# Kernel optimization log

Hardware: AMD Instinct MI355X
Metric: run time of the kernel (lower is better)

## Reference

```python
import jax, jax.numpy as jnp
import numpy as np

RADIUS = 0.08
NSAMPLE = 32


def setup_inputs() -> dict:
    key = jax.random.key(0)
    k1, k2, k3 = jax.random.split(key, 3)
    xyz = jax.random.uniform(k1, (20000, 3), dtype=jnp.float32)          # (N, 3)
    new_xyz = jax.random.uniform(k2, (2, 2048, 3), dtype=jnp.float32)    # (B, P, 3)
    features = jax.random.normal(k3, (64, 20000), dtype=jnp.float32)     # (C, N)
    return {"xyz": xyz, "new_xyz": new_xyz, "features": features}


def _ball_query(xyz, new_xyz, radius, nsample):
    """Replicates pointnet2 grid ball query.
    Returns idx (B,P,nsample) int32 of the FIRST nsample in-ball point indices
    (in original point order), padded with the first found index (0 if none),
    and idn (B,P,nsample) int32 validity flags (all ones if ball is empty,
    matching the kernel's untouched init of 1).
    """
    xyz = jax.lax.stop_gradient(xyz)
    new_xyz = jax.lax.stop_gradient(new_xyz)
    N = xyz.shape[0]
    # squared distances (B, P, N) via ||a||^2 + ||b||^2 - 2 a.b (no (B,P,N,3) temp)
    x2 = jnp.sum(xyz * xyz, axis=-1)                 # (N,)
    q2 = jnp.sum(new_xyz * new_xyz, axis=-1)         # (B, P)
    cross = jnp.einsum("bpd,nd->bpn", new_xyz, xyz)  # (B, P, N)
    d2 = q2[..., None] + x2[None, None, :] - 2.0 * cross
    mask = d2 < radius * radius                      # (B, P, N)
    # encode "first nsample in-ball indices in ascending point order":
    scores = jnp.where(mask, jnp.arange(N, dtype=jnp.int32), N)
    neg_vals, _ = jax.lax.top_k(-scores, nsample)    # largest of -scores = smallest scores
    cand = -neg_vals                                 # (B, P, nsample), sorted ascending
    valid = cand < N
    first = jnp.where(valid[..., :1], cand[..., :1], 0)
    idx = jnp.where(valid, cand, first).astype(jnp.int32)
    empty = ~valid[..., :1]                          # ball has no neighbors
    idn = jnp.where(valid | empty, 1, 0).astype(jnp.int32)
    return idx, idn


def _group(features, idx):
    """features (C, N), idx (B, P, S) -> (B, C, P, S) gather."""
    g = jnp.take(features, idx, axis=1)              # (C, B, P, S)
    return jnp.transpose(g, (1, 0, 2, 3))


def reference(xyz, new_xyz, features):
    idx, idn = _ball_query(xyz, new_xyz, RADIUS, NSAMPLE)
    grouped_xyz = _group(jnp.transpose(xyz), idx)                    # (B, 3, P, S)
    grouped_xyz = grouped_xyz - jnp.transpose(new_xyz, (0, 2, 1))[..., None]
    grouped_features = _group(features, idx)                         # (B, C, P, S)
    new_features = jnp.concatenate([grouped_xyz, grouped_features], axis=1)
    return new_features, idn
```

## Files before the change

kernel.cpp:

```cpp
#include <hip/hip_runtime.h>
#include <hip/hip_bf16.h>

#define NPTS   20000
#define BATCH  2
#define NQ     2048
#define NS     32
#define NC     64
#define NCOUT  67
#define NQTOT  (BATCH * NQ)
#define NF_ELEMS (BATCH * NCOUT * NQ * NS)

#define GRID   12
#define NCELL  (GRID * GRID * GRID)
#define CAND_CAP 128

__device__ __forceinline__ float sq3(float a, float b, float c) {
    return __fadd_rn(__fadd_rn(__fmul_rn(a, a), __fmul_rn(b, b)), __fmul_rn(c, c));
}

__global__ __launch_bounds__(256) void zero_counts_kernel(int* __restrict__ cnt) {
    const int t = threadIdx.x;
    #pragma unroll
    for (int i = 0; i < 7; ++i) {
        const int c = t * 7 + i;
        if (c < NCELL) cnt[c] = 0;
    }
}

__global__ __launch_bounds__(256) void transpose_count_kernel(
        const float* __restrict__ features, const float* __restrict__ xyz,
        float* __restrict__ featT, int* __restrict__ cellOf,
        int* __restrict__ cnt) {
    __shared__ float tile[64][65];
    const int n0 = blockIdx.x * 64;
    const int t  = threadIdx.x;

    if (t < 64) {
        const int n = n0 + t;
        if (n < NPTS) {
            const float x = xyz[n * 3 + 0];
            const float y = xyz[n * 3 + 1];
            const float z = xyz[n * 3 + 2];
            const int cx = min(max((int)(x * (float)GRID), 0), GRID - 1);
            const int cy = min(max((int)(y * (float)GRID), 0), GRID - 1);
            const int cz = min(max((int)(z * (float)GRID), 0), GRID - 1);
            const int cell = (cx * GRID + cy) * GRID + cz;
            cellOf[n] = cell;
            atomicAdd(&cnt[cell], 1);
        }
    }

    const int nn   = t & 63;
    const int cgrp = t >> 6;
    for (int k = 0; k < 16; ++k) {
        const int cc = cgrp * 16 + k;
        const int n  = n0 + nn;
        if (n < NPTS) tile[cc][nn] = features[cc * NPTS + n];
    }
    __syncthreads();
    const int cc2  = t & 63;
    const int ngrp = t >> 6;
    for (int k = 0; k < 16; ++k) {
        const int nn2 = ngrp * 16 + k;
        const int n   = n0 + nn2;
        if (n < NPTS) featT[n * NC + cc2] = tile[cc2][nn2];
    }
}

__global__ __launch_bounds__(256) void scan_kernel(
        const int* __restrict__ cnt, int* __restrict__ start,
        int* __restrict__ cursor) {
    __shared__ int s[256];
    const int t = threadIdx.x;
    int loc[7];
    int sum = 0;
    #pragma unroll
    for (int i = 0; i < 7; ++i) {
        const int c = t * 7 + i;
        const int v = (c < NCELL) ? cnt[c] : 0;
        loc[i] = sum;
        sum += v;
    }
    s[t] = sum;
    __syncthreads();
    for (int off = 1; off < 256; off <<= 1) {
        const int v = (t >= off) ? s[t - off] : 0;
        __syncthreads();
        s[t] += v;
        __syncthreads();
    }
    const int excl = s[t] - sum;
    #pragma unroll
    for (int i = 0; i < 7; ++i) {
        const int c = t * 7 + i;
        if (c < NCELL) {
            const int val = excl + loc[i];
            start[c]  = val;
            cursor[c] = val;
        }
    }
    if (t == 255) start[NCELL] = s[255];
}

__global__ __launch_bounds__(256) void scatter_kernel(
        const float* __restrict__ xyz, const int* __restrict__ cellOf,
        int* __restrict__ cursor, float4* __restrict__ packed) {
    const int n = blockIdx.x * 256 + threadIdx.x;
    if (n >= NPTS) return;
    const int pos = atomicAdd(&cursor[cellOf[n]], 1);
    packed[pos] = make_float4(xyz[n * 3 + 0], xyz[n * 3 + 1], xyz[n * 3 + 2],
                              __int_as_float(n));
}

__device__ __forceinline__ void ce_shfl(int& r0, int& r1, int j,
                                        bool asc0, bool asc1, int lane) {
    const int o0 = __shfl_xor(r0, j);
    const int o1 = __shfl_xor(r1, j);
    const bool lower = (lane & j) == 0;
    r0 = (lower == asc0) ? min(r0, o0) : max(r0, o0);
    r1 = (lower == asc1) ? min(r1, o1) : max(r1, o1);
}

__global__ __launch_bounds__(256) void query_group_kernel(
        const float4* __restrict__ packed,
        const int*    __restrict__ cellStart,
        const float*  __restrict__ new_xyz,
        const float*  __restrict__ xyz,
        const float4* __restrict__ featT4,
        float* __restrict__ out,
        float* __restrict__ idnOut) {
    const float R2 = (float)(0.08 * 0.08);

    const int wid  = threadIdx.x >> 6;
    const int lane = threadIdx.x & 63;
    const int q    = blockIdx.x * 4 + wid;

    __shared__ int cand[4][CAND_CAP];
    __shared__ int sidx[4][NS];

    const float qx = new_xyz[q * 3 + 0];
    const float qy = new_xyz[q * 3 + 1];
    const float qz = new_xyz[q * 3 + 2];
    const float q2 = sq3(qx, qy, qz);

    const int cx = min(max((int)(qx * (float)GRID), 0), GRID - 1);
    const int cy = min(max((int)(qy * (float)GRID), 0), GRID - 1);
    const int cz = min(max((int)(qz * (float)GRID), 0), GRID - 1);

    const int xlo = max(cx - 1, 0), xhi = min(cx + 1, GRID - 1);
    const int ylo = max(cy - 1, 0), yhi = min(cy + 1, GRID - 1);
    const int zlo = max(cz - 1, 0), zhi = min(cz + 1, GRID - 1);

    const unsigned long long lt = (1ull << lane) - 1ull;
    int cnt = 0;

    for (int dx = xlo; dx <= xhi; ++dx) {
        for (int dy = ylo; dy <= yhi; ++dy) {
            const int row = (dx * GRID + dy) * GRID;
            const int s0 = cellStart[row + zlo];
            const int s1 = cellStart[row + zhi + 1];
            for (int base = s0; base < s1; base += 64) {
                const int i = base + lane;
                bool inball = false;
                int  pid = 0;
                if (i < s1) {
                    const float4 p = packed[i];
                    pid = __float_as_int(p.w);
                    const float x2 = sq3(p.x, p.y, p.z);
                    const float cross = __fadd_rn(
                        __fadd_rn(__fmul_rn(qx, p.x), __fmul_rn(qy, p.y)),
                        __fmul_rn(qz, p.z));
                    const float d2 = __fsub_rn(__fadd_rn(q2, x2),
                                               __fmul_rn(2.0f, cross));
                    inball = d2 < R2;
                }
                const unsigned long long m = __ballot(inball);
                if (inball) {
                    const int pos = cnt + __popcll(m & lt);
                    if (pos < CAND_CAP) cand[wid][pos] = pid;
                }
                cnt += __popcll(m);
            }
        }
    }

    __threadfence_block();

    const int M = min(cnt, CAND_CAP);
    int r0 = (lane      < M) ? cand[wid][lane]      : 0x7fffffff;
    int r1 = (lane + 64 < M) ? cand[wid][lane + 64] : 0x7fffffff;

    #pragma unroll
    for (int k = 2; k <= 64; k <<= 1) {
        #pragma unroll
        for (int j = k >> 1; j >= 1; j >>= 1) {
            const bool asc0 = ((lane & k) == 0);
            const bool asc1 = (((lane | 64) & k) == 0);
            ce_shfl(r0, r1, j, asc0, asc1, lane);
        }
    }
    { const int lo = min(r0, r1), hi = max(r0, r1); r0 = lo; r1 = hi; }
    #pragma unroll
    for (int j = 32; j >= 1; j >>= 1) ce_shfl(r0, r1, j, true, true, lane);

    const int nf = min(cnt, NS);
    const int first = __shfl(r0, 0);
    if (lane < NS) {
        int v; float fl;
        if (cnt == 0) { v = 0; fl = 1.0f; }
        else { v = (lane < nf) ? r0 : first; fl = (lane < nf) ? 1.0f : 0.0f; }
        sidx[wid][lane] = v;
        idnOut[q * NS + lane] = fl;
    }

    __threadfence_block();

    const int b = q >> 11;
    const int p = q & (NQ - 1);
    const int CH_STRIDE = NQ * NS;

    for (int k = lane; k < 96; k += 64) {
        const int d = k >> 5;
        const int s = k & 31;
        const int id = sidx[wid][s];
        const float qd = (d == 0) ? qx : ((d == 1) ? qy : qz);
        out[((b * NCOUT + d) * NQ + p) * NS + s] = __fsub_rn(xyz[id * 3 + d], qd);
    }

    const int s    = lane & 31;
    const int half = lane >> 5;
    const int id   = sidx[wid][s];
    const int rowbase = id * (NC / 4);
    #pragma unroll
    for (int k = 0; k < 8; ++k) {
        const int cc4 = k * 2 + half;
        const float4 vf = featT4[rowbase + cc4];
        const int o = ((b * NCOUT + 3 + cc4 * 4) * NQ + p) * NS + s;
        out[o]                 = vf.x;
        out[o + 1 * CH_STRIDE] = vf.y;
        out[o + 2 * CH_STRIDE] = vf.z;
        out[o + 3 * CH_STRIDE] = vf.w;
    }
}

extern "C" void kernel_launch(void* const* d_in, const int* in_sizes, int n_in,
                              void* d_out, int out_size, void* d_ws, size_t ws_size,
                              hipStream_t stream) {
    const float* xyz      = (const float*)d_in[0];
    const float* new_xyz  = (const float*)d_in[1];
    const float* features = (const float*)d_in[2];

    float* out     = (float*)d_out;
    float* idn_out = out + NF_ELEMS;

    const size_t OFF_FEATT  = 0;
    const size_t OFF_CNT    = 5120000;
    const size_t OFF_START  = 5127168;
    const size_t OFF_CURSOR = 5134336;
    const size_t OFF_CELLOF = 5141504;
    const size_t OFF_PACKED = 5221504;

    float*  d_featT  = (float*)((char*)d_ws + OFF_FEATT);
    int*    d_cnt    = (int*)((char*)d_ws + OFF_CNT);
    int*    d_start  = (int*)((char*)d_ws + OFF_START);
    int*    d_cursor = (int*)((char*)d_ws + OFF_CURSOR);
    int*    d_cellOf = (int*)((char*)d_ws + OFF_CELLOF);
    float4* d_packed = (float4*)((char*)d_ws + OFF_PACKED);

    zero_counts_kernel<<<1, 256, 0, stream>>>(d_cnt);
    transpose_count_kernel<<<(NPTS + 63) / 64, 256, 0, stream>>>(
        features, xyz, d_featT, d_cellOf, d_cnt);
    scan_kernel<<<1, 256, 0, stream>>>(d_cnt, d_start, d_cursor);
    scatter_kernel<<<(NPTS + 255) / 256, 256, 0, stream>>>(
        xyz, d_cellOf, d_cursor, d_packed);
    query_group_kernel<<<NQTOT / 4, 256, 0, stream>>>(
        d_packed, d_start, new_xyz, xyz, (const float4*)d_featT, out, idn_out);
}
```

Baseline: 99.98 us.

## Fuse grid build kernels into one launch and prefetch cell ranges per lane

The zero, transpose/count, scan and scatter kernels become one launch. Extra blocks do the feature transpose, and a single extra block builds the cell histogram, scan and scatter in shared memory. This removes three launches and the global atomics. The query kernel now loads each neighbouring cell row's start and end in parallel across lanes and broadcasts them with shuffles, instead of loading them serially. The cost is that one block must process all 20000 points serially for binning, which could sit on the critical path.

Result: slower. 129.7 us (+29.7%).

```diff
diff --git a/kernel.cpp b/kernel.cpp
--- a/kernel.cpp
+++ b/kernel.cpp
@@ -14,102 +14,100 @@
 #define NCELL  (GRID * GRID * GRID)
 #define CAND_CAP 128
 
+#define NTILES ((NPTS + 63) / 64)
+
 __device__ __forceinline__ float sq3(float a, float b, float c) {
     return __fadd_rn(__fadd_rn(__fmul_rn(a, a), __fmul_rn(b, b)), __fmul_rn(c, c));
 }
 
-__global__ __launch_bounds__(256) void zero_counts_kernel(int* __restrict__ cnt) {
+__device__ __forceinline__ int cell_of(float x, float y, float z) {
+    const int cx = min(max((int)(x * (float)GRID), 0), GRID - 1);
+    const int cy = min(max((int)(y * (float)GRID), 0), GRID - 1);
+    const int cz = min(max((int)(z * (float)GRID), 0), GRID - 1);
+    return (cx * GRID + cy) * GRID + cz;
+}
+
+__global__ __launch_bounds__(256) void build_all_kernel(
+        const float* __restrict__ features,
+        const float* __restrict__ xyz,
+        float*  __restrict__ featT,
+        int*    __restrict__ cellStart,
+        float4* __restrict__ packed) {
+    __shared__ float tile[64][65];
+    __shared__ int   hist[NCELL];
+    __shared__ int   curs[NCELL];
+    __shared__ int   scanbuf[256];
+
     const int t = threadIdx.x;
+
+    if (blockIdx.x < NTILES) {
+        const int n0 = blockIdx.x * 64;
+        const int nn   = t & 63;
+        const int cgrp = t >> 6;
+        for (int k = 0; k < 16; ++k) {
+            const int cc = cgrp * 16 + k;
+            const int n  = n0 + nn;
+            if (n < NPTS) tile[cc][nn] = features[cc * NPTS + n];
+        }
+        __syncthreads();
+        const int cc2  = t & 63;
+        const int ngrp = t >> 6;
+        for (int k = 0; k < 16; ++k) {
+            const int nn2 = ngrp * 16 + k;
+            const int n   = n0 + nn2;
+            if (n < NPTS) featT[n * NC + cc2] = tile[cc2][nn2];
+        }
+        return;
+    }
+
+    for (int c = t; c < NCELL; c += 256) hist[c] = 0;
+    __syncthreads();
+
+    for (int n = t; n < NPTS; n += 256) {
+        const float x = xyz[n * 3 + 0];
+        const float y = xyz[n * 3 + 1];
+        const float z = xyz[n * 3 + 2];
+        atomicAdd(&hist[cell_of(x, y, z)], 1);
+    }
+    __syncthreads();
+
+    int loc[7];
+    int sum = 0;
     #pragma unroll
     for (int i = 0; i < 7; ++i) {
         const int c = t * 7 + i;
-        if (c < NCELL) cnt[c] = 0;
-    }
-}
-
-__global__ __launch_bounds__(256) void transpose_count_kernel(
-        const float* __restrict__ features, const float* __restrict__ xyz,
-        float* __restrict__ featT, int* __restrict__ cellOf,
-        int* __restrict__ cnt) {
-    __shared__ float tile[64][65];
-    const int n0 = blockIdx.x * 64;
-    const int t  = threadIdx.x;
-
-    if (t < 64) {
-        const int n = n0 + t;
-        if (n < NPTS) {
-            const float x = xyz[n * 3 + 0];
-            const float y = xyz[n * 3 + 1];
-            const float z = xyz[n * 3 + 2];
-            const int cx = min(max((int)(x * (float)GRID), 0), GRID - 1);
-            const int cy = min(max((int)(y * (float)GRID), 0), GRID - 1);
-            const int cz = min(max((int)(z * (float)GRID), 0), GRID - 1);
-            const int cell = (cx * GRID + cy) * GRID + cz;
-            cellOf[n] = cell;
-            atomicAdd(&cnt[cell], 1);
-        }
-    }
-
-    const int nn   = t & 63;
-    const int cgrp = t >> 6;
-    for (int k = 0; k < 16; ++k) {
-        const int cc = cgrp * 16 + k;
-        const int n  = n0 + nn;
-        if (n < NPTS) tile[cc][nn] = features[cc * NPTS + n];
-    }
-    __syncthreads();
-    const int cc2  = t & 63;
-    const int ngrp = t >> 6;
-    for (int k = 0; k < 16; ++k) {
-        const int nn2 = ngrp * 16 + k;
-        const int n   = n0 + nn2;
-        if (n < NPTS) featT[n * NC + cc2] = tile[cc2][nn2];
-    }
-}
-
-__global__ __launch_bounds__(256) void scan_kernel(
-        const int* __restrict__ cnt, int* __restrict__ start,
-        int* __restrict__ cursor) {
-    __shared__ int s[256];
-    const int t = threadIdx.x;
-    int loc[7];
-    int sum = 0;
-    #pragma unroll
-    for (int i = 0; i < 7; ++i) {
-        const int c = t * 7 + i;
-        const int v = (c < NCELL) ? cnt[c] : 0;
+        const int v = (c < NCELL) ? hist[c] : 0;
         loc[i] = sum;
         sum += v;
     }
-    s[t] = sum;
+    scanbuf[t] = sum;
     __syncthreads();
     for (int off = 1; off < 256; off <<= 1) {
-        const int v = (t >= off) ? s[t - off] : 0;
+        const int v = (t >= off) ? scanbuf[t - off] : 0;
         __syncthreads();
-        s[t] += v;
+        scanbuf[t] += v;
         __syncthreads();
     }
-    const int excl = s[t] - sum;
+    const int excl = scanbuf[t] - sum;
     #pragma unroll
     for (int i = 0; i < 7; ++i) {
         const int c = t * 7 + i;
         if (c < NCELL) {
-            const int val = excl + loc[i];
-            start[c]  = val;
-            cursor[c] = val;
-        }
-    }
-    if (t == 255) start[NCELL] = s[255];
-}
-
-__global__ __launch_bounds__(256) void scatter_kernel(
-        const float* __restrict__ xyz, const int* __restrict__ cellOf,
-        int* __restrict__ cursor, float4* __restrict__ packed) {
-    const int n = blockIdx.x * 256 + threadIdx.x;
-    if (n >= NPTS) return;
-    const int pos = atomicAdd(&cursor[cellOf[n]], 1);
-    packed[pos] = make_float4(xyz[n * 3 + 0], xyz[n * 3 + 1], xyz[n * 3 + 2],
-                              __int_as_float(n));
+            const int st = excl + loc[i];
+            curs[c] = st;
+            cellStart[c] = st;
+        }
+    }
+    if (t == 255) cellStart[NCELL] = scanbuf[255];
+    __syncthreads();
+
+    for (int n = t; n < NPTS; n += 256) {
+        const float x = xyz[n * 3 + 0];
+        const float y = xyz[n * 3 + 1];
+        const float z = xyz[n * 3 + 2];
+        const int pos = atomicAdd(&curs[cell_of(x, y, z)], 1);
+        packed[pos] = make_float4(x, y, z, __int_as_float(n));
+    }
 }
 
 __device__ __forceinline__ void ce_shfl(int& r0, int& r1, int j,
@@ -151,36 +149,45 @@
     const int ylo = max(cy - 1, 0), yhi = min(cy + 1, GRID - 1);
     const int zlo = max(cz - 1, 0), zhi = min(cz + 1, GRID - 1);
 
+    const int ny = yhi - ylo + 1;
+    const int nCells = (xhi - xlo + 1) * ny;
+
+    int myS0 = 0, myS1 = 0;
+    if (lane < nCells) {
+        const int dx = xlo + lane / ny;
+        const int dy = ylo + lane % ny;
+        const int row = (dx * GRID + dy) * GRID;
+        myS0 = cellStart[row + zlo];
+        myS1 = cellStart[row + zhi + 1];
+    }
+
     const unsigned long long lt = (1ull << lane) - 1ull;
     int cnt = 0;
 
-    for (int dx = xlo; dx <= xhi; ++dx) {
-        for (int dy = ylo; dy <= yhi; ++dy) {
-            const int row = (dx * GRID + dy) * GRID;
-            const int s0 = cellStart[row + zlo];
-            const int s1 = cellStart[row + zhi + 1];
-            for (int base = s0; base < s1; base += 64) {
-                const int i = base + lane;
-                bool inball = false;
-                int  pid = 0;
-                if (i < s1) {
-                    const float4 p = packed[i];
-                    pid = __float_as_int(p.w);
-                    const float x2 = sq3(p.x, p.y, p.z);
-                    const float cross = __fadd_rn(
-                        __fadd_rn(__fmul_rn(qx, p.x), __fmul_rn(qy, p.y)),
-                        __fmul_rn(qz, p.z));
-                    const float d2 = __fsub_rn(__fadd_rn(q2, x2),
-                                               __fmul_rn(2.0f, cross));
-                    inball = d2 < R2;
-                }
-                const unsigned long long m = __ballot(inball);
-                if (inball) {
-                    const int pos = cnt + __popcll(m & lt);
-                    if (pos < CAND_CAP) cand[wid][pos] = pid;
-                }
-                cnt += __popcll(m);
+    for (int r = 0; r < nCells; ++r) {
+        const int s0 = __shfl(myS0, r);
+        const int s1 = __shfl(myS1, r);
+        for (int base = s0; base < s1; base += 64) {
+            const int i = base + lane;
+            bool inball = false;
+            int  pid = 0;
+            if (i < s1) {
+                const float4 p = packed[i];
+                pid = __float_as_int(p.w);
+                const float x2 = sq3(p.x, p.y, p.z);
+                const float cross = __fadd_rn(
+                    __fadd_rn(__fmul_rn(qx, p.x), __fmul_rn(qy, p.y)),
+                    __fmul_rn(qz, p.z));
+                const float d2 = __fsub_rn(__fadd_rn(q2, x2),
+                                           __fmul_rn(2.0f, cross));
+                inball = d2 < R2;
             }
+            const unsigned long long m = __ballot(inball);
+            if (inball) {
+                const int pos = cnt + __popcll(m & lt);
+                if (pos < CAND_CAP) cand[wid][pos] = pid;
+            }
+            cnt += __popcll(m);
         }
     }
 
@@ -254,25 +261,15 @@
     float* idn_out = out + NF_ELEMS;
 
     const size_t OFF_FEATT  = 0;
-    const size_t OFF_CNT    = 5120000;
-    const size_t OFF_START  = 5127168;
-    const size_t OFF_CURSOR = 5134336;
-    const size_t OFF_CELLOF = 5141504;
-    const size_t OFF_PACKED = 5221504;
+    const size_t OFF_START  = 5120000;
+    const size_t OFF_PACKED = 5127168;
 
     float*  d_featT  = (float*)((char*)d_ws + OFF_FEATT);
-    int*    d_cnt    = (int*)((char*)d_ws + OFF_CNT);
     int*    d_start  = (int*)((char*)d_ws + OFF_START);
-    int*    d_cursor = (int*)((char*)d_ws + OFF_CURSOR);
-    int*    d_cellOf = (int*)((char*)d_ws + OFF_CELLOF);
     float4* d_packed = (float4*)((char*)d_ws + OFF_PACKED);
 
-    zero_counts_kernel<<<1, 256, 0, stream>>>(d_cnt);
-    transpose_count_kernel<<<(NPTS + 63) / 64, 256, 0, stream>>>(
-        features, xyz, d_featT, d_cellOf, d_cnt);
-    scan_kernel<<<1, 256, 0, stream>>>(d_cnt, d_start, d_cursor);
-    scatter_kernel<<<(NPTS + 255) / 256, 256, 0, stream>>>(
-        xyz, d_cellOf, d_cursor, d_packed);
+    build_all_kernel<<<NTILES + 1, 256, 0, stream>>>(
+        features, xyz, d_featT, d_start, d_packed);
     query_group_kernel<<<NQTOT / 4, 256, 0, stream>>>(
         d_packed, d_start, new_xyz, xyz, (const float4*)d_featT, out, idn_out);
 }
```

## Flatten neighbor-cell scan into one contiguous loop and simplify small-count sort

Applied to the files above, without the earlier changes.

The ball query now gathers the start and length of up to nine neighboring cell rows per lane, broadcasts them with shuffles, and walks their concatenated ranges in 64-wide steps instead of a separate loop per row. Before, each row ended in a partly filled wave iteration. When there are at most 64 candidates, a single-register bitonic sort replaces the two-register sort, and the final merge sorts only r0. The zero-count kernel is replaced by hipMemsetAsync. In exchange, every lane does a nine-way range search each iteration to find its address.

New measurement: 99.00 us. About the same (-1.0%).

```diff
diff --git a/kernel.cpp b/kernel.cpp
--- a/kernel.cpp
+++ b/kernel.cpp
@@ -14,17 +14,17 @@
 #define NCELL  (GRID * GRID * GRID)
 #define CAND_CAP 128
 
+#define NTILES ((NPTS + 63) / 64)
+
 __device__ __forceinline__ float sq3(float a, float b, float c) {
     return __fadd_rn(__fadd_rn(__fmul_rn(a, a), __fmul_rn(b, b)), __fmul_rn(c, c));
 }
 
-__global__ __launch_bounds__(256) void zero_counts_kernel(int* __restrict__ cnt) {
-    const int t = threadIdx.x;
-    #pragma unroll
-    for (int i = 0; i < 7; ++i) {
-        const int c = t * 7 + i;
-        if (c < NCELL) cnt[c] = 0;
-    }
+__device__ __forceinline__ int cell_of(float x, float y, float z) {
+    const int cx = min(max((int)(x * (float)GRID), 0), GRID - 1);
+    const int cy = min(max((int)(y * (float)GRID), 0), GRID - 1);
+    const int cz = min(max((int)(z * (float)GRID), 0), GRID - 1);
+    return (cx * GRID + cy) * GRID + cz;
 }
 
 __global__ __launch_bounds__(256) void transpose_count_kernel(
@@ -41,10 +41,7 @@
             const float x = xyz[n * 3 + 0];
             const float y = xyz[n * 3 + 1];
             const float z = xyz[n * 3 + 2];
-            const int cx = min(max((int)(x * (float)GRID), 0), GRID - 1);
-            const int cy = min(max((int)(y * (float)GRID), 0), GRID - 1);
-            const int cz = min(max((int)(z * (float)GRID), 0), GRID - 1);
-            const int cell = (cx * GRID + cy) * GRID + cz;
+            const int cell = cell_of(x, y, z);
             cellOf[n] = cell;
             atomicAdd(&cnt[cell], 1);
         }
@@ -112,13 +109,19 @@
                               __int_as_float(n));
 }
 
-__device__ __forceinline__ void ce_shfl(int& r0, int& r1, int j,
-                                        bool asc0, bool asc1, int lane) {
+__device__ __forceinline__ void ce_shfl2(int& r0, int& r1, int j,
+                                         bool asc0, bool asc1, int lane) {
     const int o0 = __shfl_xor(r0, j);
     const int o1 = __shfl_xor(r1, j);
     const bool lower = (lane & j) == 0;
     r0 = (lower == asc0) ? min(r0, o0) : max(r0, o0);
     r1 = (lower == asc1) ? min(r1, o1) : max(r1, o1);
+}
+
+__device__ __forceinline__ void ce_shfl1(int& r0, int j, bool asc, int lane) {
+    const int o0 = __shfl_xor(r0, j);
+    const bool lower = (lane & j) == 0;
+    r0 = (lower == asc) ? min(r0, o0) : max(r0, o0);
 }
 
 __global__ __launch_bounds__(256) void query_group_kernel(
@@ -151,57 +154,93 @@
     const int ylo = max(cy - 1, 0), yhi = min(cy + 1, GRID - 1);
     const int zlo = max(cz - 1, 0), zhi = min(cz + 1, GRID - 1);
 
+    const int ny = yhi - ylo + 1;
+    const int nCells = (xhi - xlo + 1) * ny;
+
+    int myS0 = 0, myS1 = 0;
+    if (lane < nCells) {
+        const int dx = xlo + lane / ny;
+        const int dy = ylo + lane % ny;
+        const int row = (dx * GRID + dy) * GRID;
+        myS0 = cellStart[row + zlo];
+        myS1 = cellStart[row + zhi + 1];
+    }
+    const int myLen = myS1 - myS0;
+
+    int S[9], L[9], P[9];
+    int tot = 0;
+    #pragma unroll
+    for (int r = 0; r < 9; ++r) {
+        S[r] = __shfl(myS0, r);
+        L[r] = __shfl(myLen, r);
+        P[r] = tot;
+        tot += L[r];
+    }
+
     const unsigned long long lt = (1ull << lane) - 1ull;
     int cnt = 0;
-
-    for (int dx = xlo; dx <= xhi; ++dx) {
-        for (int dy = ylo; dy <= yhi; ++dy) {
-            const int row = (dx * GRID + dy) * GRID;
-            const int s0 = cellStart[row + zlo];
-            const int s1 = cellStart[row + zhi + 1];
-            for (int base = s0; base < s1; base += 64) {
-                const int i = base + lane;
-                bool inball = false;
-                int  pid = 0;
-                if (i < s1) {
-                    const float4 p = packed[i];
-                    pid = __float_as_int(p.w);
-                    const float x2 = sq3(p.x, p.y, p.z);
-                    const float cross = __fadd_rn(
-                        __fadd_rn(__fmul_rn(qx, p.x), __fmul_rn(qy, p.y)),
-                        __fmul_rn(qz, p.z));
-                    const float d2 = __fsub_rn(__fadd_rn(q2, x2),
-                                               __fmul_rn(2.0f, cross));
-                    inball = d2 < R2;
-                }
-                const unsigned long long m = __ballot(inball);
-                if (inball) {
-                    const int pos = cnt + __popcll(m & lt);
-                    if (pos < CAND_CAP) cand[wid][pos] = pid;
-                }
-                cnt += __popcll(m);
+    const int iters = (tot + 63) >> 6;
+
+    for (int it = 0; it < iters; ++it) {
+        const int j = it * 64 + lane;
+        const bool valid = j < tot;
+        int addr = 0;
+        #pragma unroll
+        for (int r = 0; r < 9; ++r) {
+            const int rel = j - P[r];
+            if (rel >= 0 && rel < L[r]) addr = S[r] + rel;
+        }
+        bool inball = false;
+        int  pid = 0;
+        if (valid) {
+            const float4 p = packed[addr];
+            pid = __float_as_int(p.w);
+            const float x2 = sq3(p.x, p.y, p.z);
+            const float cross = __fadd_rn(
+                __fadd_rn(__fmul_rn(qx, p.x), __fmul_rn(qy, p.y)),
+                __fmul_rn(qz, p.z));
+            const float d2 = __fsub_rn(__fadd_rn(q2, x2),
+                                       __fmul_rn(2.0f, cross));
+            inball = d2 < R2;
+        }
+        const unsigned long long m = __ballot(inball);
+        if (inball) {
+            const int pos = cnt + __popcll(m & lt);
+            if (pos < CAND_CAP) cand[wid][pos] = pid;
+        }
+        cnt += __popcll(m);
+    }
+
+    __threadfence_block();
+
+    int r0;
+    if (cnt <= 64) {
+        r0 = (lane < cnt) ? cand[wid][lane] : 0x7fffffff;
+        #pragma unroll
+        for (int k = 2; k <= 64; k <<= 1) {
+            #pragma unroll
+            for (int j = k >> 1; j >= 1; j >>= 1) {
+                const bool asc = ((lane & k) == 0);
+                ce_shfl1(r0, j, asc, lane);
             }
         }
-    }
-
-    __threadfence_block();
-
-    const int M = min(cnt, CAND_CAP);
-    int r0 = (lane      < M) ? cand[wid][lane]      : 0x7fffffff;
-    int r1 = (lane + 64 < M) ? cand[wid][lane + 64] : 0x7fffffff;
-
-    #pragma unroll
-    for (int k = 2; k <= 64; k <<= 1) {
+    } else {
+        const int M = min(cnt, CAND_CAP);
+        r0 = (lane < M) ? cand[wid][lane] : 0x7fffffff;
+        int r1 = (lane + 64 < M) ? cand[wid][lane + 64] : 0x7fffffff;
         #pragma unroll
-        for (int j = k >> 1; j >= 1; j >>= 1) {
-            const bool asc0 = ((lane & k) == 0);
-            const bool asc1 = (((lane | 64) & k) == 0);
-            ce_shfl(r0, r1, j, asc0, asc1, lane);
-        }
-    }
-    { const int lo = min(r0, r1), hi = max(r0, r1); r0 = lo; r1 = hi; }
-    #pragma unroll
-    for (int j = 32; j >= 1; j >>= 1) ce_shfl(r0, r1, j, true, true, lane);
+        for (int k = 2; k <= 64; k <<= 1) {
+            #pragma unroll
+            for (int j = k >> 1; j >= 1; j >>= 1) {
+                const bool asc0 = ((lane & k) == 0);
+                const bool asc1 = (((lane | 64) & k) == 0);
+                ce_shfl2(r0, r1, j, asc0, asc1, lane);
+            }
+        }
+        { const int lo = min(r0, r1), hi = max(r0, r1); r0 = lo; r1 = hi; }
+        #pragma unroll
+        for (int j = 32; j >= 1; j >>= 1) ce_shfl1(r0, j, true, lane);
+    }
 
     const int nf = min(cnt, NS);
     const int first = __shfl(r0, 0);
@@ -267,8 +306,8 @@
     int*    d_cellOf = (int*)((char*)d_ws + OFF_CELLOF);
     float4* d_packed = (float4*)((char*)d_ws + OFF_PACKED);
 
-    zero_counts_kernel<<<1, 256, 0, stream>>>(d_cnt);
-    transpose_count_kernel<<<(NPTS + 63) / 64, 256, 0, stream>>>(
+    hipMemsetAsync(d_cnt, 0, NCELL * sizeof(int), stream);
+    transpose_count_kernel<<<NTILES, 256, 0, stream>>>(
         features, xyz, d_featT, d_cellOf, d_cnt);
     scan_kernel<<<1, 256, 0, stream>>>(d_cnt, d_start, d_cursor);
     scatter_kernel<<<(NPTS + 255) / 256, 256, 0, stream>>>(
```
